# Performance work log

Hardware: AMD Instinct MI355X
Metric: run time of the kernel (lower is better)

Reference implementation:

```python
import jax, jax.numpy as jnp
import numpy as np


def setup_inputs() -> dict:
    key = jax.random.key(0)
    ks = jax.random.split(key, 8)
    C, dk = 256, 32
    B, H, W = 4, 64, 64
    x = jax.random.normal(ks[0], (B, C, H, W), dtype=jnp.float32)
    wq = jax.random.normal(ks[1], (dk, C), dtype=jnp.float32) * (1.0 / np.sqrt(C))
    bq = jnp.zeros((dk,), dtype=jnp.float32)
    wk = jax.random.normal(ks[2], (dk, C), dtype=jnp.float32) * (1.0 / np.sqrt(C))
    bk = jnp.zeros((dk,), dtype=jnp.float32)
    wv = jax.random.normal(ks[3], (C, C), dtype=jnp.float32) * (1.0 / np.sqrt(C))
    bv = jnp.zeros((C,), dtype=jnp.float32)
    gamma = jnp.ones((1,), dtype=jnp.float32)
    return {"x": x, "wq": wq, "bq": bq, "wk": wk, "bk": bk,
            "wv": wv, "bv": bv, "gamma": gamma}


def reference(x, wq, bq, wk, bk, wv, bv, gamma):
    B, C, H, W = x.shape
    N = H * W
    xf = x.reshape(B, C, N)  # [B, C, N]
    # 1x1 convs == per-pixel linear projections
    q = jnp.einsum('dc,bcn->bnd', wq, xf) + bq  # [B, N, dk]  (proj_query, permuted)
    k = jnp.einsum('dc,bcn->bdn', wk, xf) + bk[None, :, None]  # [B, dk, N]
    v = jnp.einsum('ec,bcn->ben', wv, xf) + bv[None, :, None]  # [B, C, N]
    energy = jnp.einsum('bnd,bdm->bnm', q, k)  # [B, N, N]
    attention = jax.nn.softmax(energy, axis=-1)
    # out[b,c,i] = sum_j v[b,c,j] * attention[b,i,j]
    out = jnp.einsum('bcj,bij->bci', v, attention)  # [B, C, N]
    out = out.reshape(B, C, H, W)
    return gamma[0] * out + x
```

## Files before the change

### kernel.cpp

```cpp
#include <hip/hip_runtime.h>
#include <hip/hip_bf16.h>

#define NPIX 4096
#define CIN  256
#define DK   32

typedef __attribute__((ext_vector_type(8))) short short8;
typedef __attribute__((ext_vector_type(16))) float f32x16;

__device__ __forceinline__ unsigned short f2bf(float f) {
    unsigned int u = __float_as_uint(f);
    return (unsigned short)((u + 0x7fffu + ((u >> 16) & 1u)) >> 16);
}
__device__ __forceinline__ float bf2f(unsigned short h) {
    return __uint_as_float(((unsigned int)h) << 16);
}
__device__ __forceinline__ unsigned int f2bf2(float a, float b) {
    __hip_bfloat162 h = __float22bfloat162_rn(make_float2(a, b));
    unsigned int u;
    __builtin_memcpy(&u, &h, 4);
    return u;
}

__global__ void wprep_kernel(const float* __restrict__ wq, const float* __restrict__ wk,
                             const float* __restrict__ wv,
                             unsigned short* __restrict__ wqh, unsigned short* __restrict__ wql,
                             unsigned short* __restrict__ wkh, unsigned short* __restrict__ wkl,
                             unsigned short* __restrict__ wvh) {
    const int lane = threadIdx.x & 63, li = lane & 31, hi = lane >> 5;
    const int kc = blockIdx.x, y = blockIdx.y;
    if (y < 4) {
        const float* m = (y < 2) ? wq : wk;
        short8 h8, l8;
#pragma unroll
        for (int e = 0; e < 8; ++e) {
            float v = m[li * CIN + kc * 16 + hi * 8 + e];
            unsigned short hb = f2bf(v);
            h8[e] = (short)hb;
            l8[e] = (short)f2bf(v - bf2f(hb));
        }
        unsigned short* dst = (y == 0) ? wqh : (y == 1) ? wql : (y == 2) ? wkh : wkl;
        *reinterpret_cast<short8*>(&dst[kc * 512 + lane * 8]) = (y & 1) ? l8 : h8;
    } else {
        const int cblk = y - 4;
        short8 h8;
#pragma unroll
        for (int e = 0; e < 8; ++e)
            h8[e] = (short)f2bf(wv[(cblk * 32 + li) * CIN + kc * 16 + hi * 8 + e]);
        *reinterpret_cast<short8*>(&wvh[(cblk * 16 + kc) * 512 + lane * 8]) = h8;
    }
}

__global__ __launch_bounds__(512) void projall_kernel(
        const float* __restrict__ x,
        const unsigned short* __restrict__ wqh, const unsigned short* __restrict__ wql,
        const unsigned short* __restrict__ wkh, const unsigned short* __restrict__ wkl,
        const unsigned short* __restrict__ wvh,
        const float* __restrict__ bq, const float* __restrict__ bk, const float* __restrict__ bv,
        unsigned short* __restrict__ qfrag, unsigned short* __restrict__ kfrag,
        unsigned short* __restrict__ vfrag) {
    __shared__ unsigned short ts[2][32][40];

    const int t = threadIdx.x, lane = t & 63, li = lane & 31, hi = lane >> 5, w = t >> 6;
    const int nblk = blockIdx.x, b = blockIdx.y;
    const int n0 = nblk * 32;
    const float* xb = x + (size_t)(b * CIN + hi * 8) * NPIX + n0 + li;

    if (w < 2) {
        const unsigned short* wh = (w == 0) ? wqh : wkh;
        const unsigned short* wl = (w == 0) ? wql : wkl;
        const float* bias = (w == 0) ? bq : bk;
        f32x16 acc;
#pragma unroll
        for (int r = 0; r < 16; ++r) acc[r] = 0.f;
        for (int kc = 0; kc < 16; ++kc) {
            short8 ah, al;
#pragma unroll
            for (int e = 0; e < 8; ++e) {
                float v = xb[(size_t)(kc * 16 + e) * NPIX];
                unsigned short hb = f2bf(v);
                ah[e] = (short)hb;
                al[e] = (short)f2bf(v - bf2f(hb));
            }
            short8 whf = *reinterpret_cast<const short8*>(&wh[kc * 512 + lane * 8]);
            short8 wlf = *reinterpret_cast<const short8*>(&wl[kc * 512 + lane * 8]);
            acc = __builtin_amdgcn_mfma_f32_32x32x16_bf16(ah, whf, acc, 0, 0, 0);
            acc = __builtin_amdgcn_mfma_f32_32x32x16_bf16(al, whf, acc, 0, 0, 0);
            acc = __builtin_amdgcn_mfma_f32_32x32x16_bf16(ah, wlf, acc, 0, 0, 0);
        }
        const float bs = bias[li];
#pragma unroll
        for (int r = 0; r < 16; ++r) {
            int row = (r & 3) + 8 * (r >> 2) + 4 * hi;
            ts[w][row][li] = f2bf(acc[r] + bs);
        }
        unsigned short* dstf = (w == 0) ? qfrag : kfrag;
#pragma unroll
        for (int dh = 0; dh < 2; ++dh) {
            short8 f = *reinterpret_cast<const short8*>(&ts[w][li][dh * 16 + hi * 8]);
            *reinterpret_cast<short8*>(
                &dstf[((size_t)(b * 128 + nblk) * 2 + dh) * 512 + lane * 8]) = f;
        }
    } else {
        const int w2 = w - 2;
        const int njob = (w2 < 2) ? 2 : 1;
        for (int jj = 0; jj < njob; ++jj) {
            const int cblk = w2 + jj * 6;
            f32x16 acc;
#pragma unroll
            for (int r = 0; r < 16; ++r) acc[r] = 0.f;
            for (int kc = 0; kc < 16; ++kc) {
                short8 xf;
#pragma unroll
                for (int e = 0; e < 8; ++e)
                    xf[e] = (short)f2bf(xb[(size_t)(kc * 16 + e) * NPIX]);
                short8 wf = *reinterpret_cast<const short8*>(&wvh[(cblk * 16 + kc) * 512 + lane * 8]);
                acc = __builtin_amdgcn_mfma_f32_32x32x16_bf16(xf, wf, acc, 0, 0, 0);
            }
            const float bvv = bv[cblk * 32 + li];
#pragma unroll
            for (int g = 0; g < 2; ++g) {
                short8 sv;
#pragma unroll
                for (int e = 0; e < 8; ++e) sv[e] = (short)f2bf(acc[g * 8 + e] + bvv);
                *reinterpret_cast<short8*>(
                    &vfrag[((size_t)(b * 8 + cblk) * 256 + nblk * 2 + g) * 512 + lane * 8]) = sv;
            }
        }
    }
}

__global__ __launch_bounds__(512, 4) void attnv_kernel(
        const unsigned short* __restrict__ qfrag, const unsigned short* __restrict__ kfrag,
        const unsigned short* __restrict__ vfrag, unsigned short* __restrict__ opart,
        float* __restrict__ lpart, float* __restrict__ out) {
    __shared__ unsigned short Ps[4 * 8 * 512];
    __shared__ float sred[2][4][32];

    const int t = threadIdx.x, lane = t & 63, li = lane & 31, hi = lane >> 5, w = t >> 6;
    const int blk = blockIdx.x;
    const int xcd = blk & 7, slot = blk >> 3;
    const int jh = slot & 1, ps = slot >> 1;
    const int b = xcd >> 1;
    const int ipos = (xcd & 1) * 32 + ps;
    const int it = w >> 2, sl = w & 3;
    const int cq = w;

    short8 qb0, qb1;
    {
        size_t qoff = ((size_t)(b * 128 + ipos * 2 + it) * 2) * 512 + lane * 8;
        qb0 = *reinterpret_cast<const short8*>(&qfrag[qoff]);
        qb1 = *reinterpret_cast<const short8*>(&qfrag[qoff + 512]);
    }
    float ssum = 0.f;

    f32x16 acc0, acc1;
#pragma unroll
    for (int r = 0; r < 16; ++r) { acc0[r] = 0.f; acc1[r] = 0.f; }

    short8 kp0, kp1;
    short8 vp[8];

    auto kload = [&](int s) {
        size_t koff = ((size_t)(b * 128 + jh * 64 + s * 4 + sl) * 2) * 512 + lane * 8;
        kp0 = *reinterpret_cast<const short8*>(&kfrag[koff]);
        kp1 = *reinterpret_cast<const short8*>(&kfrag[koff + 512]);
    };
    auto vload = [&](int s) {
        size_t vb = ((size_t)(b * 8 + cq) * 256 + jh * 128 + s * 8) * 512 + lane * 8;
#pragma unroll
        for (int kc = 0; kc < 8; ++kc)
            vp[kc] = *reinterpret_cast<const short8*>(&vfrag[vb + kc * 512]);
    };
    auto do_E = [&](int s) {
        f32x16 e;
#pragma unroll
        for (int r = 0; r < 16; ++r) e[r] = 0.f;
        e = __builtin_amdgcn_mfma_f32_32x32x16_bf16(kp0, qb0, e, 0, 0, 0);
        e = __builtin_amdgcn_mfma_f32_32x32x16_bf16(kp1, qb1, e, 0, 0, 0);
        const int buf = s & 1;
#pragma unroll
        for (int g = 0; g < 2; ++g) {
            float p0 = __expf(e[g * 8 + 0]), p1 = __expf(e[g * 8 + 1]);
            float p2 = __expf(e[g * 8 + 2]), p3 = __expf(e[g * 8 + 3]);
            float p4 = __expf(e[g * 8 + 4]), p5 = __expf(e[g * 8 + 5]);
            float p6 = __expf(e[g * 8 + 6]), p7 = __expf(e[g * 8 + 7]);
            ssum += ((p0 + p1) + (p2 + p3)) + ((p4 + p5) + (p6 + p7));
            uint4 pk;
            pk.x = f2bf2(p0, p1); pk.y = f2bf2(p2, p3);
            pk.z = f2bf2(p4, p5); pk.w = f2bf2(p6, p7);
            *reinterpret_cast<uint4*>(
                &Ps[((it * 2 + buf) * 8 + sl * 2 + g) * 512 + lane * 8]) = pk;
        }
    };

    kload(0);
    vload(0);
    do_E(0);
    kload(1);
    __syncthreads();

#pragma unroll 1
    for (int s = 0; s < 16; ++s) {
        if (s + 1 < 16) {
            do_E(s + 1);
            if (s + 2 < 16) kload(s + 2);
        }
        const int buf = s & 1;
#pragma unroll
        for (int kc = 0; kc < 8; ++kc) {
            short8 B0 = *reinterpret_cast<const short8*>(&Ps[(buf * 8 + kc) * 512 + lane * 8]);
            short8 B1 = *reinterpret_cast<const short8*>(&Ps[((2 + buf) * 8 + kc) * 512 + lane * 8]);
            acc0 = __builtin_amdgcn_mfma_f32_32x32x16_bf16(vp[kc], B0, acc0, 0, 0, 0);
            acc1 = __builtin_amdgcn_mfma_f32_32x32x16_bf16(vp[kc], B1, acc1, 0, 0, 0);
        }
        if (s + 1 < 16) vload(s + 1);
        __syncthreads();
    }

    ssum += __shfl_xor(ssum, 32);
    if (lane < 32) sred[it][sl][li] = ssum;
    __syncthreads();
    if (sl == 0 && lane < 32) {
        float lt = sred[it][0][li] + sred[it][1][li] + sred[it][2][li] + sred[it][3][li];
        lpart[((size_t)jh * 4 + b) * NPIX + ipos * 64 + it * 32 + li] = lt;
    }

#pragma unroll
    for (int itt = 0; itt < 2; ++itt) {
        const f32x16& A = itt ? acc1 : acc0;
#pragma unroll
        for (int r = 0; r < 16; ++r) {
            int c = cq * 32 + (r & 3) + 8 * (r >> 2) + 4 * hi;
            size_t idx = (size_t)(b * CIN + c) * NPIX + ipos * 64 + itt * 32 + li;
            if (jh == 0) out[idx] = A[r];
            else         opart[idx] = f2bf(A[r]);
        }
    }
}

__global__ __launch_bounds__(256) void merge_kernel(
        const unsigned short* __restrict__ opart, const float* __restrict__ lpart,
        const float* __restrict__ xin, const float* __restrict__ gamma,
        float* __restrict__ out) {
    const size_t idx8 = ((size_t)blockIdx.x * 256 + threadIdx.x) * 8;
    const size_t i  = idx8 & (NPIX - 1);
    const size_t b  = idx8 >> 20;
    short8 o1v = *reinterpret_cast<const short8*>(&opart[idx8]);
    float4 o00 = *reinterpret_cast<const float4*>(&out[idx8]);
    float4 o01 = *reinterpret_cast<const float4*>(&out[idx8 + 4]);
    float4 x0  = *reinterpret_cast<const float4*>(&xin[idx8]);
    float4 x1  = *reinterpret_cast<const float4*>(&xin[idx8 + 4]);
    float4 la0 = *reinterpret_cast<const float4*>(&lpart[b * NPIX + i]);
    float4 la1 = *reinterpret_cast<const float4*>(&lpart[b * NPIX + i + 4]);
    float4 lb0 = *reinterpret_cast<const float4*>(&lpart[(4 + b) * NPIX + i]);
    float4 lb1 = *reinterpret_cast<const float4*>(&lpart[(4 + b) * NPIX + i + 4]);
    const float g = gamma[0];
    float4 o;
    o.x = g * (o00.x + bf2f((unsigned short)o1v[0])) / (la0.x + lb0.x) + x0.x;
    o.y = g * (o00.y + bf2f((unsigned short)o1v[1])) / (la0.y + lb0.y) + x0.y;
    o.z = g * (o00.z + bf2f((unsigned short)o1v[2])) / (la0.z + lb0.z) + x0.z;
    o.w = g * (o00.w + bf2f((unsigned short)o1v[3])) / (la0.w + lb0.w) + x0.w;
    *reinterpret_cast<float4*>(&out[idx8]) = o;
    o.x = g * (o01.x + bf2f((unsigned short)o1v[4])) / (la1.x + lb1.x) + x1.x;
    o.y = g * (o01.y + bf2f((unsigned short)o1v[5])) / (la1.y + lb1.y) + x1.y;
    o.z = g * (o01.z + bf2f((unsigned short)o1v[6])) / (la1.z + lb1.z) + x1.z;
    o.w = g * (o01.w + bf2f((unsigned short)o1v[7])) / (la1.w + lb1.w) + x1.w;
    *reinterpret_cast<float4*>(&out[idx8 + 4]) = o;
}

extern "C" void kernel_launch(void* const* d_in, const int* in_sizes, int n_in,
                              void* d_out, int out_size, void* d_ws, size_t ws_size,
                              hipStream_t stream) {
    const float* x     = (const float*)d_in[0];
    const float* wq    = (const float*)d_in[1];
    const float* bq    = (const float*)d_in[2];
    const float* wk    = (const float*)d_in[3];
    const float* bk    = (const float*)d_in[4];
    const float* wv    = (const float*)d_in[5];
    const float* bv    = (const float*)d_in[6];
    const float* gamma = (const float*)d_in[7];
    float* out = (float*)d_out;

    unsigned short* qf    = (unsigned short*)d_ws;
    unsigned short* kf    = qf + (size_t)524288;
    unsigned short* vf    = kf + (size_t)524288;
    unsigned short* wqh   = vf + (size_t)4194304;
    unsigned short* wql   = wqh + 8192;
    unsigned short* wkh   = wql + 8192;
    unsigned short* wkl   = wkh + 8192;
    unsigned short* wvh   = wkl + 8192;
    unsigned short* opart = wvh + 65536;
    float*          lpart = (float*)(opart + 4194304);

    wprep_kernel<<<dim3(16, 12), 64, 0, stream>>>(wq, wk, wv, wqh, wql, wkh, wkl, wvh);
    projall_kernel<<<dim3(128, 4), 512, 0, stream>>>(x, wqh, wql, wkh, wkl, wvh,
                                                     bq, bk, bv, qf, kf, vf);
    attnv_kernel<<<dim3(512), 512, 0, stream>>>(qf, kf, vf, opart, lpart, out);
    merge_kernel<<<dim3(2048), 256, 0, stream>>>(opart, lpart, x, gamma, out);
}
```

Before: 147.8 us.

## Stage x in LDS for projections and deepen attention P buffering

The projection kernel now loads each 32-pixel x tile once into shared memory with coalesced float4 loads. It converts the tile to bf16 hi/lo MFMA fragments there, so all warps share them instead of each warp reloading and re-converting x from global memory. The attention kernel grows the P scratch from two to four buffers per row tile, computes energies two steps ahead, and places barriers only on every other iteration. It also interleaves the next V fragment loads with the MFMAs. The trade-off is that the P buffer doubles to 64KB of LDS, which may cut resident blocks per CU below the launch-bounds target of 4.

```diff
diff --git a/kernel.cpp b/kernel.cpp
--- a/kernel.cpp
+++ b/kernel.cpp
@@ -59,12 +59,39 @@
         const float* __restrict__ bq, const float* __restrict__ bk, const float* __restrict__ bv,
         unsigned short* __restrict__ qfrag, unsigned short* __restrict__ kfrag,
         unsigned short* __restrict__ vfrag) {
+    __shared__ float xs[64][36];
+    __shared__ unsigned short xhf[16 * 512];
+    __shared__ unsigned short xlf[16 * 512];
     __shared__ unsigned short ts[2][32][40];
 
     const int t = threadIdx.x, lane = t & 63, li = lane & 31, hi = lane >> 5, w = t >> 6;
     const int nblk = blockIdx.x, b = blockIdx.y;
     const int n0 = nblk * 32;
-    const float* xb = x + (size_t)(b * CIN + hi * 8) * NPIX + n0 + li;
+
+    for (int cb = 0; cb < 4; ++cb) {
+        {
+            int c = t >> 3, n4 = (t & 7) * 4;
+            float4 v = *reinterpret_cast<const float4*>(
+                &x[(size_t)(b * CIN + cb * 64 + c) * NPIX + n0 + n4]);
+            xs[c][n4 + 0] = v.x; xs[c][n4 + 1] = v.y;
+            xs[c][n4 + 2] = v.z; xs[c][n4 + 3] = v.w;
+        }
+        __syncthreads();
+        {
+            const int kc = w & 3;
+            const bool isL = (w >= 4);
+            short8 f;
+#pragma unroll
+            for (int e = 0; e < 8; ++e) {
+                float v = xs[kc * 16 + hi * 8 + e][li];
+                unsigned short hb = f2bf(v);
+                f[e] = isL ? (short)f2bf(v - bf2f(hb)) : (short)hb;
+            }
+            unsigned short* dst = isL ? xlf : xhf;
+            *reinterpret_cast<short8*>(&dst[(cb * 4 + kc) * 512 + lane * 8]) = f;
+        }
+        __syncthreads();
+    }
 
     if (w < 2) {
         const unsigned short* wh = (w == 0) ? wqh : wkh;
@@ -74,14 +101,8 @@
 #pragma unroll
         for (int r = 0; r < 16; ++r) acc[r] = 0.f;
         for (int kc = 0; kc < 16; ++kc) {
-            short8 ah, al;
-#pragma unroll
-            for (int e = 0; e < 8; ++e) {
-                float v = xb[(size_t)(kc * 16 + e) * NPIX];
-                unsigned short hb = f2bf(v);
-                ah[e] = (short)hb;
-                al[e] = (short)f2bf(v - bf2f(hb));
-            }
+            short8 ah = *reinterpret_cast<const short8*>(&xhf[kc * 512 + lane * 8]);
+            short8 al = *reinterpret_cast<const short8*>(&xlf[kc * 512 + lane * 8]);
             short8 whf = *reinterpret_cast<const short8*>(&wh[kc * 512 + lane * 8]);
             short8 wlf = *reinterpret_cast<const short8*>(&wl[kc * 512 + lane * 8]);
             acc = __builtin_amdgcn_mfma_f32_32x32x16_bf16(ah, whf, acc, 0, 0, 0);
@@ -110,12 +131,9 @@
 #pragma unroll
             for (int r = 0; r < 16; ++r) acc[r] = 0.f;
             for (int kc = 0; kc < 16; ++kc) {
-                short8 xf;
-#pragma unroll
-                for (int e = 0; e < 8; ++e)
-                    xf[e] = (short)f2bf(xb[(size_t)(kc * 16 + e) * NPIX]);
+                short8 xb = *reinterpret_cast<const short8*>(&xhf[kc * 512 + lane * 8]);
                 short8 wf = *reinterpret_cast<const short8*>(&wvh[(cblk * 16 + kc) * 512 + lane * 8]);
-                acc = __builtin_amdgcn_mfma_f32_32x32x16_bf16(xf, wf, acc, 0, 0, 0);
+                acc = __builtin_amdgcn_mfma_f32_32x32x16_bf16(xb, wf, acc, 0, 0, 0);
             }
             const float bvv = bv[cblk * 32 + li];
 #pragma unroll
@@ -134,7 +152,7 @@
         const unsigned short* __restrict__ qfrag, const unsigned short* __restrict__ kfrag,
         const unsigned short* __restrict__ vfrag, unsigned short* __restrict__ opart,
         float* __restrict__ lpart, float* __restrict__ out) {
-    __shared__ unsigned short Ps[4 * 8 * 512];
+    __shared__ unsigned short Ps[8 * 8 * 512];
     __shared__ float sred[2][4][32];
 
     const int t = threadIdx.x, lane = t & 63, li = lane & 31, hi = lane >> 5, w = t >> 6;
@@ -158,27 +176,21 @@
 #pragma unroll
     for (int r = 0; r < 16; ++r) { acc0[r] = 0.f; acc1[r] = 0.f; }
 
-    short8 kp0, kp1;
+    short8 kp[2][2];
     short8 vp[8];
 
     auto kload = [&](int s) {
         size_t koff = ((size_t)(b * 128 + jh * 64 + s * 4 + sl) * 2) * 512 + lane * 8;
-        kp0 = *reinterpret_cast<const short8*>(&kfrag[koff]);
-        kp1 = *reinterpret_cast<const short8*>(&kfrag[koff + 512]);
-    };
-    auto vload = [&](int s) {
-        size_t vb = ((size_t)(b * 8 + cq) * 256 + jh * 128 + s * 8) * 512 + lane * 8;
-#pragma unroll
-        for (int kc = 0; kc < 8; ++kc)
-            vp[kc] = *reinterpret_cast<const short8*>(&vfrag[vb + kc * 512]);
+        kp[s & 1][0] = *reinterpret_cast<const short8*>(&kfrag[koff]);
+        kp[s & 1][1] = *reinterpret_cast<const short8*>(&kfrag[koff + 512]);
     };
     auto do_E = [&](int s) {
         f32x16 e;
 #pragma unroll
         for (int r = 0; r < 16; ++r) e[r] = 0.f;
-        e = __builtin_amdgcn_mfma_f32_32x32x16_bf16(kp0, qb0, e, 0, 0, 0);
-        e = __builtin_amdgcn_mfma_f32_32x32x16_bf16(kp1, qb1, e, 0, 0, 0);
-        const int buf = s & 1;
+        e = __builtin_amdgcn_mfma_f32_32x32x16_bf16(kp[s & 1][0], qb0, e, 0, 0, 0);
+        e = __builtin_amdgcn_mfma_f32_32x32x16_bf16(kp[s & 1][1], qb1, e, 0, 0, 0);
+        const int buf = s & 3;
 #pragma unroll
         for (int g = 0; g < 2; ++g) {
             float p0 = __expf(e[g * 8 + 0]), p1 = __expf(e[g * 8 + 1]);
@@ -190,32 +202,42 @@
             pk.x = f2bf2(p0, p1); pk.y = f2bf2(p2, p3);
             pk.z = f2bf2(p4, p5); pk.w = f2bf2(p6, p7);
             *reinterpret_cast<uint4*>(
-                &Ps[((it * 2 + buf) * 8 + sl * 2 + g) * 512 + lane * 8]) = pk;
+                &Ps[((it * 4 + buf) * 8 + sl * 2 + g) * 512 + lane * 8]) = pk;
         }
     };
-
-    kload(0);
-    vload(0);
-    do_E(0);
-    kload(1);
+    auto vbase = [&](int s) {
+        return ((size_t)(b * 8 + cq) * 256 + jh * 128 + s * 8) * 512 + lane * 8;
+    };
+
+    kload(0); do_E(0);
+    kload(1); do_E(1);
+    {
+        size_t vb = vbase(0);
+#pragma unroll
+        for (int kc = 0; kc < 8; ++kc)
+            vp[kc] = *reinterpret_cast<const short8*>(&vfrag[vb + kc * 512]);
+    }
+    kload(2); kload(3);
     __syncthreads();
 
 #pragma unroll 1
     for (int s = 0; s < 16; ++s) {
-        if (s + 1 < 16) {
-            do_E(s + 1);
-            if (s + 2 < 16) kload(s + 2);
-        }
-        const int buf = s & 1;
+        if (s + 2 < 16) {
+            do_E(s + 2);
+            if (s + 4 < 16) kload(s + 4);
+        }
+        const int buf = s & 3;
+        const size_t vbn = (s + 1 < 16) ? vbase(s + 1) : 0;
 #pragma unroll
         for (int kc = 0; kc < 8; ++kc) {
             short8 B0 = *reinterpret_cast<const short8*>(&Ps[(buf * 8 + kc) * 512 + lane * 8]);
-            short8 B1 = *reinterpret_cast<const short8*>(&Ps[((2 + buf) * 8 + kc) * 512 + lane * 8]);
+            short8 B1 = *reinterpret_cast<const short8*>(&Ps[((4 + buf) * 8 + kc) * 512 + lane * 8]);
             acc0 = __builtin_amdgcn_mfma_f32_32x32x16_bf16(vp[kc], B0, acc0, 0, 0, 0);
             acc1 = __builtin_amdgcn_mfma_f32_32x32x16_bf16(vp[kc], B1, acc1, 0, 0, 0);
-        }
-        if (s + 1 < 16) vload(s + 1);
-        __syncthreads();
+            if (s + 1 < 16)
+                vp[kc] = *reinterpret_cast<const short8*>(&vfrag[vbn + kc * 512]);
+        }
+        if (s & 1) __syncthreads();
     }
 
     ssum += __shfl_xor(ssum, 32);
```

Result: slower. 479.7 us (+224.5%).
